# Kernel optimization log

Hardware: AMD Instinct MI355X
Metric: run time of the kernel (lower is better)

The kernel has to match this reference:

```python
import jax, jax.numpy as jnp
import numpy as np

B, C, H, W = 64, 256, 16, 16
HEADS, HEAD_DIM = 8, 256            # NOTE: source code requires H*W == HEAD_DIM
HID = HEADS * HEAD_DIM              # 2048
TEMB = 512
EPS = 1e-6
SC = HEAD_DIM ** -0.5


def setup_inputs() -> dict:
    key = jax.random.key(0)
    ks = jax.random.split(key, 6)
    return {
        "x": jax.random.normal(ks[0], (B, C, H, W), jnp.float32),
        "time_emb": jax.random.normal(ks[1], (B, TEMB), jnp.float32),
        "mlp_w": jax.random.normal(ks[2], (2 * C, TEMB), jnp.float32) * 0.02,
        "mlp_b": jnp.zeros((2 * C,), jnp.float32),
        "qkv_w": jax.random.normal(ks[3], (3 * HID, C), jnp.float32) * 0.02,
        "out_w": jax.random.normal(ks[4], (C, HID), jnp.float32) * 0.02,
        "out_b": jnp.zeros((C,), jnp.float32),
        "out_norm_scale": jnp.ones((C,), jnp.float32),
    }


def reference(x, time_emb, mlp_w, mlp_b, qkv_w, out_w, out_b, out_norm_scale):
    # AdaRMSNorm: SiLU -> Linear -> per-batch (scale, shift) over channels
    ss = jax.nn.silu(time_emb) @ mlp_w.T + mlp_b          # [B, 2C]
    scale, shift = jnp.split(ss, 2, axis=1)
    scale = scale[:, :, None, None]
    shift = shift[:, :, None, None]
    inv = jax.lax.rsqrt(jnp.mean(x * x, axis=1, keepdims=True) + EPS)
    xn = x * inv * (1.0 + scale) + shift

    # 1x1 conv producing q,k,v
    qkv = jnp.einsum('bchw,oc->bohw', xn, qkv_w)          # [B, 3*HID, H, W]
    q, k, v = jnp.split(qkv, 3, axis=1)

    def to_heads(t):
        return t.reshape(B, HEADS, HEAD_DIM, H * W)       # [B, h, d, L]

    q = jax.nn.softmax(to_heads(q), axis=2) * SC          # softmax over head_dim
    k = jax.nn.softmax(to_heads(k), axis=3)               # softmax over spatial
    v = to_heads(v)

    # Faithful to source einsums (contract over head_dim c, then over c and lw1)
    ctx = jnp.einsum('bhcn,bhcm->bhnm', k, v) * SC        # [B, h, L, L]
    out = jnp.einsum('bhnm,bhcl->bhml', ctx, q)           # [B, h, L, L]

    # rearrange 'b h c (l w) -> b (h c) l w' (valid since L == HEAD_DIM)
    out = out.reshape(B, HID, H, W)

    # output 1x1 conv + RMSNorm + residual
    y = jnp.einsum('bohw,co->bchw', out, out_w) + out_b[None, :, None, None]
    inv2 = jax.lax.rsqrt(jnp.mean(y * y, axis=1, keepdims=True) + EPS)
    y = y * inv2 * out_norm_scale[None, :, None, None]
    return y + x
```

## Files before the change

### kernel.cpp

```cpp
#include <hip/hip_runtime.h>
#include <math.h>


static constexpr float EPSV = 1e-6f;
static constexpr float SC2 = 1.0f / 256.0f;

__device__ __forceinline__ float wave_sum(float v) {
    v += __shfl_xor(v, 1);  v += __shfl_xor(v, 2);
    v += __shfl_xor(v, 4);  v += __shfl_xor(v, 8);
    v += __shfl_xor(v, 16); v += __shfl_xor(v, 32);
    return v;
}

__global__ void __launch_bounds__(256) k0_prep(
    const float* __restrict__ temb, const float* __restrict__ mlp_w,
    const float* __restrict__ mlp_b, const float* __restrict__ qkv_w,
    float* __restrict__ scsh, float* __restrict__ wvg)
{
    const int blk = blockIdx.x, tid = threadIdx.x;
    const int wv = tid >> 6, lane = tid & 63;
    if (blk < 1024) {
        int b = blk >> 4, jg = blk & 15;
        __shared__ float sl[512];
        float v0 = temb[b * 512 + tid];
        float v1 = temb[b * 512 + 256 + tid];
        sl[tid] = v0 / (1.0f + expf(-v0));
        sl[256 + tid] = v1 / (1.0f + expf(-v1));
        __syncthreads();
        int j0 = jg * 32 + wv * 8;
        float acc[8] = {0, 0, 0, 0, 0, 0, 0, 0};
        const float* wb = mlp_w + (size_t)j0 * 512 + lane;
#pragma unroll
        for (int k = 0; k < 8; ++k) {
            float sv = sl[k * 64 + lane];
#pragma unroll
            for (int jj = 0; jj < 8; ++jj)
                acc[jj] = fmaf(wb[(size_t)jj * 512 + k * 64], sv, acc[jj]);
        }
#pragma unroll
        for (int jj = 0; jj < 8; ++jj) {
            float a = wave_sum(acc[jj]);
            if (lane == 0) scsh[b * 512 + j0 + jj] = a + mlp_b[j0 + jj];
        }
    } else {
        int w = blk - 1024;
        int h = w >> 2, cq = w & 3;
        __shared__ float sm[256];
        const float* base =
            qkv_w + (size_t)(4096 + h * 256 + wv * 64) * 256 + cq * 64 + lane;
        float s = 0.f;
#pragma unroll 8
        for (int r = 0; r < 64; ++r) s += base[(size_t)r * 256];
        sm[wv * 64 + lane] = s;
        __syncthreads();
        if (tid < 64)
            wvg[h * 256 + cq * 64 + tid] =
                sm[tid] + sm[64 + tid] + sm[128 + tid] + sm[192 + tid];
    }
}

__global__ void __launch_bounds__(1024) k1_body(
    const float* __restrict__ x, const float* __restrict__ scsh,
    const float* __restrict__ wvg, const float* __restrict__ out_w,
    float* __restrict__ ypart)
{
    const int blk = blockIdx.x, tid = threadIdx.x;
    const int wv = tid >> 6, lane = tid & 63;
    const int b = blk >> 2, q = blk & 3;

    __shared__ float coef[256 * 8];
    __shared__ float apart[16 * 64 * 9];
    __shared__ float ofl[512];
    __shared__ float ssh[8];
    __shared__ float parts[4 * 8];

    if (tid < 256) {
        int c = tid;
        float sc = 1.0f + scsh[b * 512 + c];
        float sh = scsh[b * 512 + 256 + c];
#pragma unroll
        for (int h = 0; h < 8; ++h) {
            float wvv = wvg[h * 256 + c];
            coef[c * 8 + h] = sc * wvv;
            float sv = wave_sum(sh * wvv);
            if (lane == 0) parts[wv * 8 + h] = sv;
        }
    }
    __syncthreads();
    if (tid < 8)
        ssh[tid] = parts[tid] + parts[8 + tid] + parts[16 + tid] + parts[24 + tid];

    {
        int m = tid & 63, cg = tid >> 6;
        float A[8] = {0, 0, 0, 0, 0, 0, 0, 0};
        float ss2 = 0.f;
        const float* xb = x + (size_t)b * 65536 + q * 64 + m;
#pragma unroll
        for (int ci = 0; ci < 16; ++ci) {
            int c = cg * 16 + ci;
            float xv = xb[(size_t)c * 256];
            ss2 = fmaf(xv, xv, ss2);
            const float4 c0 = *reinterpret_cast<const float4*>(&coef[c * 8]);
            const float4 c1 = *reinterpret_cast<const float4*>(&coef[c * 8 + 4]);
            A[0] = fmaf(xv, c0.x, A[0]); A[1] = fmaf(xv, c0.y, A[1]);
            A[2] = fmaf(xv, c0.z, A[2]); A[3] = fmaf(xv, c0.w, A[3]);
            A[4] = fmaf(xv, c1.x, A[4]); A[5] = fmaf(xv, c1.y, A[5]);
            A[6] = fmaf(xv, c1.z, A[6]); A[7] = fmaf(xv, c1.w, A[7]);
        }
        float* ap = apart + ((size_t)(tid >> 6) * 64 + m) * 9;
#pragma unroll
        for (int h = 0; h < 8; ++h) ap[h] = A[h];
        ap[8] = ss2;
        (void)cg;
    }
    __syncthreads();
    if (tid < 64) {
        int m = tid;
        float fin[9] = {0, 0, 0, 0, 0, 0, 0, 0, 0};
#pragma unroll
        for (int g = 0; g < 16; ++g)
#pragma unroll
            for (int i = 0; i < 9; ++i)
                fin[i] += apart[((size_t)g * 64 + m) * 9 + i];
        float inv = rsqrtf(fin[8] * (1.0f / 256.0f) + EPSV);
#pragma unroll
        for (int h = 0; h < 8; ++h)
            ofl[h * 64 + m] = SC2 * fmaf(inv, fin[h], ssh[h]);
    }
    __syncthreads();

    const float4* of4 = reinterpret_cast<const float4*>(ofl);
#pragma unroll
    for (int g4 = 0; g4 < 4; ++g4) {
        int c0 = wv * 16 + g4 * 4;
        float a[4] = {0, 0, 0, 0};
#pragma unroll
        for (int cc = 0; cc < 4; ++cc) {
            int c = c0 + cc;
#pragma unroll
            for (int k = 0; k < 2; ++k) {
                int idx = k * 64 + lane;
                int h = idx >> 4, mm = (idx & 15) * 4;
                const float4 w4 = *reinterpret_cast<const float4*>(
                    &out_w[(size_t)c * 2048 + h * 256 + q * 64 + mm]);
                float4 ov = of4[idx];
                a[cc] = fmaf(w4.x, ov.x, a[cc]);
                a[cc] = fmaf(w4.y, ov.y, a[cc]);
                a[cc] = fmaf(w4.z, ov.z, a[cc]);
                a[cc] = fmaf(w4.w, ov.w, a[cc]);
            }
        }
#pragma unroll
        for (int cc = 0; cc < 4; ++cc) {
            float s = wave_sum(a[cc]);
            if (lane == 0) ypart[(size_t)q * 16384 + b * 256 + c0 + cc] = s;
        }
    }
}

__global__ void __launch_bounds__(256) k2_fin(
    const float* __restrict__ ypart, const float* __restrict__ out_b,
    const float* __restrict__ onorm, const float* __restrict__ x,
    float* __restrict__ out)
{
    const int blk = blockIdx.x, tid = threadIdx.x;
    const int b = blk >> 5, ch = blk & 31;
    __shared__ float gl[256];
    __shared__ float wred[4];
    float yb = out_b[tid] +
               ypart[b * 256 + tid] + ypart[16384 + b * 256 + tid] +
               ypart[32768 + b * 256 + tid] + ypart[49152 + b * 256 + tid];
    float v2 = wave_sum(yb * yb);
    if ((tid & 63) == 0) wred[tid >> 6] = v2;
    __syncthreads();
    float inv2 = rsqrtf((wred[0] + wred[1] + wred[2] + wred[3]) *
                        (1.0f / 256.0f) + EPSV);
    gl[tid] = yb * inv2 * onorm[tid];
    __syncthreads();

    const float4* xx = reinterpret_cast<const float4*>(x) +
                       (size_t)b * 16384 + ch * 512;
    float4* oo = reinterpret_cast<float4*>(out) + (size_t)b * 16384 + ch * 512;
#pragma unroll
    for (int k = 0; k < 2; ++k) {
        int i = k * 256 + tid;
        int row = (ch * 512 + i) >> 6;
        float4 xv = xx[i];
        float gg = gl[row];
        oo[i] = make_float4(xv.x + gg, xv.y + gg, xv.z + gg, xv.w + gg);
    }
}

extern "C" void kernel_launch(void* const* d_in, const int* in_sizes, int n_in,
                              void* d_out, int out_size, void* d_ws, size_t ws_size,
                              hipStream_t stream) {
    const float* x     = (const float*)d_in[0];
    const float* temb  = (const float*)d_in[1];
    const float* mlp_w = (const float*)d_in[2];
    const float* mlp_b = (const float*)d_in[3];
    const float* qkv_w = (const float*)d_in[4];
    const float* out_w = (const float*)d_in[5];
    const float* out_b = (const float*)d_in[6];
    const float* onorm = (const float*)d_in[7];
    float* out = (float*)d_out;
    float* ws  = (float*)d_ws;

    float* scsh  = ws;
    float* wvg   = ws + 32768;
    float* ypart = ws + 34816;

    k0_prep<<<1056, 256,  0, stream>>>(temb, mlp_w, mlp_b, qkv_w, scsh, wvg);
    k1_body<<<256,  1024, 0, stream>>>(x, scsh, wvg, out_w, ypart);
    k2_fin <<<2048, 256,  0, stream>>>(ypart, out_b, onorm, x, out);
}
```

Before: 35.02 us.

## Fuse three kernels into one persistent kernel with inter-block flag synchronization

Merges the prep, body and finalize kernels into a single 256-block launch. Blocks publish completion flags in workspace with release atomics and spin on them with acquire loads, replacing the kernel boundaries. A memset clears the flags before each launch. This removes two launch gaps and intermediate scheduling overhead, but the kernel depends on all 256 blocks being co-resident (otherwise it can deadlock), adds a memset, and loses parallelism in the prep and final phases.

Result: slower. 49.14 us (+40.3%).

```diff
diff --git a/kernel.cpp b/kernel.cpp
--- a/kernel.cpp
+++ b/kernel.cpp
@@ -4,6 +4,8 @@
 
 static constexpr float EPSV = 1e-6f;
 static constexpr float SC2 = 1.0f / 256.0f;
+
+#define NTHR 1024
 
 __device__ __forceinline__ float wave_sum(float v) {
     v += __shfl_xor(v, 1);  v += __shfl_xor(v, 2);
@@ -12,22 +14,40 @@
     return v;
 }
 
-__global__ void __launch_bounds__(256) k0_prep(
-    const float* __restrict__ temb, const float* __restrict__ mlp_w,
-    const float* __restrict__ mlp_b, const float* __restrict__ qkv_w,
-    float* __restrict__ scsh, float* __restrict__ wvg)
+__device__ __forceinline__ void rel_flag(unsigned* f) {
+    __hip_atomic_store(f, 1u, __ATOMIC_RELEASE, __HIP_MEMORY_SCOPE_AGENT);
+}
+__device__ __forceinline__ void spin_flag(unsigned* f) {
+    while (!__hip_atomic_load(f, __ATOMIC_RELAXED, __HIP_MEMORY_SCOPE_AGENT))
+        __builtin_amdgcn_s_sleep(1);
+    (void)__hip_atomic_load(f, __ATOMIC_ACQUIRE, __HIP_MEMORY_SCOPE_AGENT);
+}
+
+__global__ void __launch_bounds__(NTHR) k_all(
+    const float* __restrict__ x, const float* __restrict__ temb,
+    const float* __restrict__ mlp_w, const float* __restrict__ mlp_b,
+    const float* __restrict__ qkv_w, const float* __restrict__ out_w,
+    const float* __restrict__ out_b, const float* __restrict__ onorm,
+    float* __restrict__ out, float* __restrict__ ws)
 {
+    __shared__ float smem[12288];
+    unsigned* uf = (unsigned*)ws;
+    float* scsh  = ws + 16384;
+    float* wvg   = ws + 49152;
+    float* ypart = ws + 51200;
+
     const int blk = blockIdx.x, tid = threadIdx.x;
     const int wv = tid >> 6, lane = tid & 63;
-    if (blk < 1024) {
-        int b = blk >> 4, jg = blk & 15;
-        __shared__ float sl[512];
-        float v0 = temb[b * 512 + tid];
-        float v1 = temb[b * 512 + 256 + tid];
-        sl[tid] = v0 / (1.0f + expf(-v0));
-        sl[256 + tid] = v1 / (1.0f + expf(-v1));
-        __syncthreads();
-        int j0 = jg * 32 + wv * 8;
+    const int b = blk >> 2, q = blk & 3;
+
+    {
+        float* sl = smem;
+        if (tid < 512) {
+            float v = temb[b * 512 + tid];
+            sl[tid] = v / (1.0f + expf(-v));
+        }
+        __syncthreads();
+        int j0 = q * 128 + wv * 8;
         float acc[8] = {0, 0, 0, 0, 0, 0, 0, 0};
         const float* wb = mlp_w + (size_t)j0 * 512 + lane;
 #pragma unroll
@@ -42,37 +62,36 @@
             float a = wave_sum(acc[jj]);
             if (lane == 0) scsh[b * 512 + j0 + jj] = a + mlp_b[j0 + jj];
         }
-    } else {
-        int w = blk - 1024;
-        int h = w >> 2, cq = w & 3;
-        __shared__ float sm[256];
-        const float* base =
-            qkv_w + (size_t)(4096 + h * 256 + wv * 64) * 256 + cq * 64 + lane;
-        float s = 0.f;
-#pragma unroll 8
-        for (int r = 0; r < 64; ++r) s += base[(size_t)r * 256];
-        sm[wv * 64 + lane] = s;
-        __syncthreads();
-        if (tid < 64)
-            wvg[h * 256 + cq * 64 + tid] =
-                sm[tid] + sm[64 + tid] + sm[128 + tid] + sm[192 + tid];
-    }
-}
-
-__global__ void __launch_bounds__(1024) k1_body(
-    const float* __restrict__ x, const float* __restrict__ scsh,
-    const float* __restrict__ wvg, const float* __restrict__ out_w,
-    float* __restrict__ ypart)
-{
-    const int blk = blockIdx.x, tid = threadIdx.x;
-    const int wv = tid >> 6, lane = tid & 63;
-    const int b = blk >> 2, q = blk & 3;
-
-    __shared__ float coef[256 * 8];
-    __shared__ float apart[16 * 64 * 9];
-    __shared__ float ofl[512];
-    __shared__ float ssh[8];
-    __shared__ float parts[4 * 8];
+        if (blk < 32) {
+            int h = blk >> 2, cq = blk & 3;
+            float* wsum = smem + 512;
+            const float* base = qkv_w +
+                (size_t)(4096 + h * 256 + wv * 16) * 256 + cq * 64 + lane;
+            float s = 0.f;
+#pragma unroll
+            for (int r = 0; r < 16; ++r) s += base[(size_t)r * 256];
+            wsum[wv * 64 + lane] = s;
+            __syncthreads();
+            if (tid < 64) {
+                float t = 0.f;
+#pragma unroll
+                for (int r = 0; r < 16; ++r) t += wsum[r * 64 + tid];
+                wvg[h * 256 + cq * 64 + tid] = t;
+            }
+        }
+        __syncthreads();
+        if (tid == 0) rel_flag(uf + blk * 16);
+    }
+
+    if (tid < 4) spin_flag(uf + (b * 4 + tid) * 16);
+    else if (tid >= 64 && tid < 96) spin_flag(uf + (tid - 64) * 16);
+    __syncthreads();
+
+    float* coef  = smem;
+    float* apart = smem + 2048;
+    float* ofl   = smem + 11264;
+    float* ssh   = smem + 11776;
+    float* parts = smem + 11784;
 
     if (tid < 256) {
         int c = tid;
@@ -107,11 +126,10 @@
             A[4] = fmaf(xv, c1.x, A[4]); A[5] = fmaf(xv, c1.y, A[5]);
             A[6] = fmaf(xv, c1.z, A[6]); A[7] = fmaf(xv, c1.w, A[7]);
         }
-        float* ap = apart + ((size_t)(tid >> 6) * 64 + m) * 9;
+        float* ap = apart + ((size_t)cg * 64 + m) * 9;
 #pragma unroll
         for (int h = 0; h < 8; ++h) ap[h] = A[h];
         ap[8] = ss2;
-        (void)cg;
     }
     __syncthreads();
     if (tid < 64) {
@@ -129,65 +147,70 @@
     }
     __syncthreads();
 
-    const float4* of4 = reinterpret_cast<const float4*>(ofl);
-#pragma unroll
-    for (int g4 = 0; g4 < 4; ++g4) {
-        int c0 = wv * 16 + g4 * 4;
-        float a[4] = {0, 0, 0, 0};
-#pragma unroll
-        for (int cc = 0; cc < 4; ++cc) {
-            int c = c0 + cc;
-#pragma unroll
-            for (int k = 0; k < 2; ++k) {
-                int idx = k * 64 + lane;
-                int h = idx >> 4, mm = (idx & 15) * 4;
-                const float4 w4 = *reinterpret_cast<const float4*>(
-                    &out_w[(size_t)c * 2048 + h * 256 + q * 64 + mm]);
-                float4 ov = of4[idx];
-                a[cc] = fmaf(w4.x, ov.x, a[cc]);
-                a[cc] = fmaf(w4.y, ov.y, a[cc]);
-                a[cc] = fmaf(w4.z, ov.z, a[cc]);
-                a[cc] = fmaf(w4.w, ov.w, a[cc]);
+    {
+        const float4* of4 = reinterpret_cast<const float4*>(ofl);
+#pragma unroll
+        for (int g4 = 0; g4 < 4; ++g4) {
+            int c0 = wv * 16 + g4 * 4;
+            float a[4] = {0, 0, 0, 0};
+#pragma unroll
+            for (int cc = 0; cc < 4; ++cc) {
+                int c = c0 + cc;
+#pragma unroll
+                for (int k = 0; k < 2; ++k) {
+                    int idx = k * 64 + lane;
+                    int h = idx >> 4, mm = (idx & 15) * 4;
+                    const float4 w4 = *reinterpret_cast<const float4*>(
+                        &out_w[(size_t)c * 2048 + h * 256 + q * 64 + mm]);
+                    float4 ov = of4[idx];
+                    a[cc] = fmaf(w4.x, ov.x, a[cc]);
+                    a[cc] = fmaf(w4.y, ov.y, a[cc]);
+                    a[cc] = fmaf(w4.z, ov.z, a[cc]);
+                    a[cc] = fmaf(w4.w, ov.w, a[cc]);
+                }
             }
-        }
-#pragma unroll
-        for (int cc = 0; cc < 4; ++cc) {
-            float s = wave_sum(a[cc]);
-            if (lane == 0) ypart[(size_t)q * 16384 + b * 256 + c0 + cc] = s;
-        }
-    }
-}
-
-__global__ void __launch_bounds__(256) k2_fin(
-    const float* __restrict__ ypart, const float* __restrict__ out_b,
-    const float* __restrict__ onorm, const float* __restrict__ x,
-    float* __restrict__ out)
-{
-    const int blk = blockIdx.x, tid = threadIdx.x;
-    const int b = blk >> 5, ch = blk & 31;
-    __shared__ float gl[256];
-    __shared__ float wred[4];
-    float yb = out_b[tid] +
-               ypart[b * 256 + tid] + ypart[16384 + b * 256 + tid] +
-               ypart[32768 + b * 256 + tid] + ypart[49152 + b * 256 + tid];
-    float v2 = wave_sum(yb * yb);
-    if ((tid & 63) == 0) wred[tid >> 6] = v2;
-    __syncthreads();
-    float inv2 = rsqrtf((wred[0] + wred[1] + wred[2] + wred[3]) *
-                        (1.0f / 256.0f) + EPSV);
-    gl[tid] = yb * inv2 * onorm[tid];
-    __syncthreads();
-
-    const float4* xx = reinterpret_cast<const float4*>(x) +
-                       (size_t)b * 16384 + ch * 512;
-    float4* oo = reinterpret_cast<float4*>(out) + (size_t)b * 16384 + ch * 512;
-#pragma unroll
-    for (int k = 0; k < 2; ++k) {
-        int i = k * 256 + tid;
-        int row = (ch * 512 + i) >> 6;
-        float4 xv = xx[i];
-        float gg = gl[row];
-        oo[i] = make_float4(xv.x + gg, xv.y + gg, xv.z + gg, xv.w + gg);
+#pragma unroll
+            for (int cc = 0; cc < 4; ++cc) {
+                float s = wave_sum(a[cc]);
+                if (lane == 0)
+                    ypart[(size_t)q * 16384 + b * 256 + c0 + cc] = s;
+            }
+        }
+        __syncthreads();
+        if (tid == 0) rel_flag(uf + 4096 + blk * 16);
+    }
+
+    if (tid < 4) spin_flag(uf + 4096 + (b * 4 + tid) * 16);
+    __syncthreads();
+
+    {
+        float* g    = smem;
+        float* wred = smem + 320;
+        float yb = 0.f;
+        if (tid < 256) {
+            yb = out_b[tid] +
+                 ypart[b * 256 + tid] + ypart[16384 + b * 256 + tid] +
+                 ypart[32768 + b * 256 + tid] + ypart[49152 + b * 256 + tid];
+            float v2 = wave_sum(yb * yb);
+            if (lane == 0) wred[wv] = v2;
+        }
+        __syncthreads();
+        float inv2 = rsqrtf((wred[0] + wred[1] + wred[2] + wred[3]) *
+                            (1.0f / 256.0f) + EPSV);
+        if (tid < 256) g[tid] = yb * inv2 * onorm[tid];
+        __syncthreads();
+
+        const float4* xx = reinterpret_cast<const float4*>(x) + (size_t)b * 16384;
+        float4* oo = reinterpret_cast<float4*>(out) + (size_t)b * 16384;
+#pragma unroll
+        for (int r = 0; r < 4; ++r) {
+            int c = r * 64 + (tid >> 4);
+            int i = tid & 15;
+            size_t idx = (size_t)c * 64 + q * 16 + i;
+            float4 xv = xx[idx];
+            float gg = g[c];
+            oo[idx] = make_float4(xv.x + gg, xv.y + gg, xv.z + gg, xv.w + gg);
+        }
     }
 }
 
@@ -205,11 +228,7 @@
     float* out = (float*)d_out;
     float* ws  = (float*)d_ws;
 
-    float* scsh  = ws;
-    float* wvg   = ws + 32768;
-    float* ypart = ws + 34816;
-
-    k0_prep<<<1056, 256,  0, stream>>>(temb, mlp_w, mlp_b, qkv_w, scsh, wvg);
-    k1_body<<<256,  1024, 0, stream>>>(x, scsh, wvg, out_w, ypart);
-    k2_fin <<<2048, 256,  0, stream>>>(ypart, out_b, onorm, x, out);
-}
+    hipMemsetAsync(ws, 0, 32768, stream);
+    k_all<<<256, NTHR, 0, stream>>>(x, temb, mlp_w, mlp_b, qkv_w,
+                                    out_w, out_b, onorm, out, ws);
+}
```

## Fuse final RMSNorm and residual kernel into body kernel via inter-block flags

Applied to the files above, without the earlier changes.

Drops the separate finalize kernel. Each body block publishes its partial output-conv results, raises a release flag, then spins until the other three blocks of the same batch have done the same. It then computes the output RMSNorm and writes its quarter of the residual output. This removes one kernel launch and a round trip of the partials, but adds a hipMemsetAsync to clear the flags. It also relies on all 256 blocks being co-resident, or the spin-wait can deadlock.

After: 40.94 us. 16.9% more time.

```diff
diff --git a/kernel.cpp b/kernel.cpp
--- a/kernel.cpp
+++ b/kernel.cpp
@@ -10,6 +10,15 @@
     v += __shfl_xor(v, 4);  v += __shfl_xor(v, 8);
     v += __shfl_xor(v, 16); v += __shfl_xor(v, 32);
     return v;
+}
+
+__device__ __forceinline__ void rel_flag(unsigned* f) {
+    __hip_atomic_store(f, 1u, __ATOMIC_RELEASE, __HIP_MEMORY_SCOPE_AGENT);
+}
+__device__ __forceinline__ void spin_flag(unsigned* f) {
+    while (!__hip_atomic_load(f, __ATOMIC_RELAXED, __HIP_MEMORY_SCOPE_AGENT))
+        __builtin_amdgcn_s_sleep(1);
+    (void)__hip_atomic_load(f, __ATOMIC_ACQUIRE, __HIP_MEMORY_SCOPE_AGENT);
 }
 
 __global__ void __launch_bounds__(256) k0_prep(
@@ -62,11 +71,15 @@
 __global__ void __launch_bounds__(1024) k1_body(
     const float* __restrict__ x, const float* __restrict__ scsh,
     const float* __restrict__ wvg, const float* __restrict__ out_w,
-    float* __restrict__ ypart)
+    const float* __restrict__ out_b, const float* __restrict__ onorm,
+    float* __restrict__ out, float* __restrict__ ws)
 {
     const int blk = blockIdx.x, tid = threadIdx.x;
     const int wv = tid >> 6, lane = tid & 63;
     const int b = blk >> 2, q = blk & 3;
+
+    unsigned* uf = (unsigned*)ws;
+    float* ypart = ws + 4096;
 
     __shared__ float coef[256 * 8];
     __shared__ float apart[16 * 64 * 9];
@@ -107,11 +120,10 @@
             A[4] = fmaf(xv, c1.x, A[4]); A[5] = fmaf(xv, c1.y, A[5]);
             A[6] = fmaf(xv, c1.z, A[6]); A[7] = fmaf(xv, c1.w, A[7]);
         }
-        float* ap = apart + ((size_t)(tid >> 6) * 64 + m) * 9;
+        float* ap = apart + ((size_t)cg * 64 + m) * 9;
 #pragma unroll
         for (int h = 0; h < 8; ++h) ap[h] = A[h];
         ap[8] = ss2;
-        (void)cg;
     }
     __syncthreads();
     if (tid < 64) {
@@ -129,65 +141,70 @@
     }
     __syncthreads();
 
-    const float4* of4 = reinterpret_cast<const float4*>(ofl);
-#pragma unroll
-    for (int g4 = 0; g4 < 4; ++g4) {
-        int c0 = wv * 16 + g4 * 4;
-        float a[4] = {0, 0, 0, 0};
-#pragma unroll
-        for (int cc = 0; cc < 4; ++cc) {
-            int c = c0 + cc;
-#pragma unroll
-            for (int k = 0; k < 2; ++k) {
-                int idx = k * 64 + lane;
-                int h = idx >> 4, mm = (idx & 15) * 4;
-                const float4 w4 = *reinterpret_cast<const float4*>(
-                    &out_w[(size_t)c * 2048 + h * 256 + q * 64 + mm]);
-                float4 ov = of4[idx];
-                a[cc] = fmaf(w4.x, ov.x, a[cc]);
-                a[cc] = fmaf(w4.y, ov.y, a[cc]);
-                a[cc] = fmaf(w4.z, ov.z, a[cc]);
-                a[cc] = fmaf(w4.w, ov.w, a[cc]);
+    {
+        const float4* of4 = reinterpret_cast<const float4*>(ofl);
+#pragma unroll
+        for (int g4 = 0; g4 < 4; ++g4) {
+            int c0 = wv * 16 + g4 * 4;
+            float a[4] = {0, 0, 0, 0};
+#pragma unroll
+            for (int cc = 0; cc < 4; ++cc) {
+                int c = c0 + cc;
+#pragma unroll
+                for (int k = 0; k < 2; ++k) {
+                    int idx = k * 64 + lane;
+                    int h = idx >> 4, mm = (idx & 15) * 4;
+                    const float4 w4 = *reinterpret_cast<const float4*>(
+                        &out_w[(size_t)c * 2048 + h * 256 + q * 64 + mm]);
+                    float4 ov = of4[idx];
+                    a[cc] = fmaf(w4.x, ov.x, a[cc]);
+                    a[cc] = fmaf(w4.y, ov.y, a[cc]);
+                    a[cc] = fmaf(w4.z, ov.z, a[cc]);
+                    a[cc] = fmaf(w4.w, ov.w, a[cc]);
+                }
             }
-        }
-#pragma unroll
-        for (int cc = 0; cc < 4; ++cc) {
-            float s = wave_sum(a[cc]);
-            if (lane == 0) ypart[(size_t)q * 16384 + b * 256 + c0 + cc] = s;
-        }
-    }
-}
-
-__global__ void __launch_bounds__(256) k2_fin(
-    const float* __restrict__ ypart, const float* __restrict__ out_b,
-    const float* __restrict__ onorm, const float* __restrict__ x,
-    float* __restrict__ out)
-{
-    const int blk = blockIdx.x, tid = threadIdx.x;
-    const int b = blk >> 5, ch = blk & 31;
-    __shared__ float gl[256];
-    __shared__ float wred[4];
-    float yb = out_b[tid] +
-               ypart[b * 256 + tid] + ypart[16384 + b * 256 + tid] +
-               ypart[32768 + b * 256 + tid] + ypart[49152 + b * 256 + tid];
-    float v2 = wave_sum(yb * yb);
-    if ((tid & 63) == 0) wred[tid >> 6] = v2;
-    __syncthreads();
-    float inv2 = rsqrtf((wred[0] + wred[1] + wred[2] + wred[3]) *
-                        (1.0f / 256.0f) + EPSV);
-    gl[tid] = yb * inv2 * onorm[tid];
-    __syncthreads();
-
-    const float4* xx = reinterpret_cast<const float4*>(x) +
-                       (size_t)b * 16384 + ch * 512;
-    float4* oo = reinterpret_cast<float4*>(out) + (size_t)b * 16384 + ch * 512;
-#pragma unroll
-    for (int k = 0; k < 2; ++k) {
-        int i = k * 256 + tid;
-        int row = (ch * 512 + i) >> 6;
-        float4 xv = xx[i];
-        float gg = gl[row];
-        oo[i] = make_float4(xv.x + gg, xv.y + gg, xv.z + gg, xv.w + gg);
+#pragma unroll
+            for (int cc = 0; cc < 4; ++cc) {
+                float s = wave_sum(a[cc]);
+                if (lane == 0)
+                    ypart[(size_t)q * 16384 + b * 256 + c0 + cc] = s;
+            }
+        }
+    }
+    __syncthreads();
+    if (tid == 0) rel_flag(uf + blk * 16);
+
+    if (tid < 4) spin_flag(uf + (b * 4 + tid) * 16);
+    __syncthreads();
+
+    {
+        float* g    = coef;
+        float* wred = coef + 320;
+        float yb = 0.f;
+        if (tid < 256) {
+            yb = out_b[tid] +
+                 ypart[b * 256 + tid] + ypart[16384 + b * 256 + tid] +
+                 ypart[32768 + b * 256 + tid] + ypart[49152 + b * 256 + tid];
+            float v2 = wave_sum(yb * yb);
+            if (lane == 0) wred[wv] = v2;
+        }
+        __syncthreads();
+        float inv2 = rsqrtf((wred[0] + wred[1] + wred[2] + wred[3]) *
+                            (1.0f / 256.0f) + EPSV);
+        if (tid < 256) g[tid] = yb * inv2 * onorm[tid];
+        __syncthreads();
+
+        const float4* xx = reinterpret_cast<const float4*>(x) + (size_t)b * 16384;
+        float4* oo = reinterpret_cast<float4*>(out) + (size_t)b * 16384;
+#pragma unroll
+        for (int r = 0; r < 4; ++r) {
+            int c = r * 64 + (tid >> 4);
+            int i = tid & 15;
+            size_t idx = (size_t)c * 64 + q * 16 + i;
+            float4 xv = xx[idx];
+            float gg = g[c];
+            oo[idx] = make_float4(xv.x + gg, xv.y + gg, xv.z + gg, xv.w + gg);
+        }
     }
 }
 
@@ -205,11 +222,11 @@
     float* out = (float*)d_out;
     float* ws  = (float*)d_ws;
 
-    float* scsh  = ws;
-    float* wvg   = ws + 32768;
-    float* ypart = ws + 34816;
-
+    float* scsh = ws + 69632;
+    float* wvg  = ws + 102400;
+
+    hipMemsetAsync(ws, 0, 16384, stream);
     k0_prep<<<1056, 256,  0, stream>>>(temb, mlp_w, mlp_b, qkv_w, scsh, wvg);
-    k1_body<<<256,  1024, 0, stream>>>(x, scsh, wvg, out_w, ypart);
-    k2_fin <<<2048, 256,  0, stream>>>(ypart, out_b, onorm, x, out);
-}
+    k1_body<<<256,  1024, 0, stream>>>(x, scsh, wvg, out_w, out_b, onorm,
+                                       out, ws);
+}
```

## Split k1 body into 512 blocks over 32-column spatial chunks

Applied to the files above, without the earlier changes.

Doubles the k1 grid from 256 to 512 blocks by splitting each batch's spatial positions into 8 chunks of 32 instead of 4 chunks of 64. The channel reduction is reworked so 288 threads sum the partials in parallel instead of 64 threads doing it serially, and all 1024 threads now build the coefficient table. The output projection keeps each thread's ofl values in registers. The aim is to fill more compute units and cut the serial reduction, at the cost of more ypart partials for k2 to sum and more total reads of out_w.

Result: slower. 37.21 us (+6.3%).

```diff
diff --git a/kernel.cpp b/kernel.cpp
--- a/kernel.cpp
+++ b/kernel.cpp
@@ -66,38 +66,41 @@
 {
     const int blk = blockIdx.x, tid = threadIdx.x;
     const int wv = tid >> 6, lane = tid & 63;
-    const int b = blk >> 2, q = blk & 3;
+    const int b = blk >> 3, oc = blk & 7;
 
     __shared__ float coef[256 * 8];
-    __shared__ float apart[16 * 64 * 9];
-    __shared__ float ofl[512];
+    __shared__ float apart[32 * 32 * 9];
+    __shared__ float finbuf[32 * 9];
+    __shared__ float ofl[256];
     __shared__ float ssh[8];
-    __shared__ float parts[4 * 8];
-
-    if (tid < 256) {
-        int c = tid;
+    __shared__ float parts[8 * 4];
+
+    {
+        int c = tid & 255, hp = tid >> 8;
         float sc = 1.0f + scsh[b * 512 + c];
         float sh = scsh[b * 512 + 256 + c];
 #pragma unroll
-        for (int h = 0; h < 8; ++h) {
+        for (int e = 0; e < 2; ++e) {
+            int h = hp * 2 + e;
             float wvv = wvg[h * 256 + c];
             coef[c * 8 + h] = sc * wvv;
             float sv = wave_sum(sh * wvv);
-            if (lane == 0) parts[wv * 8 + h] = sv;
+            if (lane == 0) parts[h * 4 + (wv & 3)] = sv;
         }
     }
     __syncthreads();
     if (tid < 8)
-        ssh[tid] = parts[tid] + parts[8 + tid] + parts[16 + tid] + parts[24 + tid];
+        ssh[tid] = parts[tid * 4 + 0] + parts[tid * 4 + 1] +
+                   parts[tid * 4 + 2] + parts[tid * 4 + 3];
 
     {
-        int m = tid & 63, cg = tid >> 6;
+        int m = tid & 31, cg = tid >> 5;
         float A[8] = {0, 0, 0, 0, 0, 0, 0, 0};
         float ss2 = 0.f;
-        const float* xb = x + (size_t)b * 65536 + q * 64 + m;
-#pragma unroll
-        for (int ci = 0; ci < 16; ++ci) {
-            int c = cg * 16 + ci;
+        const float* xb = x + (size_t)b * 65536 + oc * 32 + m;
+#pragma unroll
+        for (int ci = 0; ci < 8; ++ci) {
+            int c = cg * 8 + ci;
             float xv = xb[(size_t)c * 256];
             ss2 = fmaf(xv, xv, ss2);
             const float4 c0 = *reinterpret_cast<const float4*>(&coef[c * 8]);
@@ -107,53 +110,54 @@
             A[4] = fmaf(xv, c1.x, A[4]); A[5] = fmaf(xv, c1.y, A[5]);
             A[6] = fmaf(xv, c1.z, A[6]); A[7] = fmaf(xv, c1.w, A[7]);
         }
-        float* ap = apart + ((size_t)(tid >> 6) * 64 + m) * 9;
+        float* ap = apart + ((size_t)cg * 32 + m) * 9;
 #pragma unroll
         for (int h = 0; h < 8; ++h) ap[h] = A[h];
         ap[8] = ss2;
-        (void)cg;
-    }
-    __syncthreads();
-    if (tid < 64) {
-        int m = tid;
-        float fin[9] = {0, 0, 0, 0, 0, 0, 0, 0, 0};
-#pragma unroll
-        for (int g = 0; g < 16; ++g)
-#pragma unroll
-            for (int i = 0; i < 9; ++i)
-                fin[i] += apart[((size_t)g * 64 + m) * 9 + i];
-        float inv = rsqrtf(fin[8] * (1.0f / 256.0f) + EPSV);
-#pragma unroll
-        for (int h = 0; h < 8; ++h)
-            ofl[h * 64 + m] = SC2 * fmaf(inv, fin[h], ssh[h]);
-    }
-    __syncthreads();
-
-    const float4* of4 = reinterpret_cast<const float4*>(ofl);
-#pragma unroll
-    for (int g4 = 0; g4 < 4; ++g4) {
-        int c0 = wv * 16 + g4 * 4;
-        float a[4] = {0, 0, 0, 0};
-#pragma unroll
-        for (int cc = 0; cc < 4; ++cc) {
-            int c = c0 + cc;
-#pragma unroll
-            for (int k = 0; k < 2; ++k) {
-                int idx = k * 64 + lane;
-                int h = idx >> 4, mm = (idx & 15) * 4;
+    }
+    __syncthreads();
+
+    if (tid < 288) {
+        int m = tid & 31, i = tid >> 5;
+        float s = 0.f;
+#pragma unroll
+        for (int cg = 0; cg < 32; ++cg)
+            s += apart[((size_t)cg * 32 + m) * 9 + i];
+        finbuf[m * 9 + i] = s;
+    }
+    __syncthreads();
+
+    if (tid < 256) {
+        int h = tid >> 5, m = tid & 31;
+        float inv = rsqrtf(finbuf[m * 9 + 8] * (1.0f / 256.0f) + EPSV);
+        ofl[h * 32 + m] = SC2 * fmaf(inv, finbuf[m * 9 + h], ssh[h]);
+    }
+    __syncthreads();
+
+    {
+        const float4* of4 = reinterpret_cast<const float4*>(ofl);
+        int h = lane >> 3, mm4 = lane & 7;
+        const float4 ov = of4[lane];
+        const size_t wbase = (size_t)h * 256 + oc * 32 + mm4 * 4;
+#pragma unroll
+        for (int g4 = 0; g4 < 4; ++g4) {
+            int c0 = wv * 16 + g4 * 4;
+            float a[4] = {0, 0, 0, 0};
+#pragma unroll
+            for (int cc = 0; cc < 4; ++cc) {
                 const float4 w4 = *reinterpret_cast<const float4*>(
-                    &out_w[(size_t)c * 2048 + h * 256 + q * 64 + mm]);
-                float4 ov = of4[idx];
+                    &out_w[(size_t)(c0 + cc) * 2048 + wbase]);
                 a[cc] = fmaf(w4.x, ov.x, a[cc]);
                 a[cc] = fmaf(w4.y, ov.y, a[cc]);
                 a[cc] = fmaf(w4.z, ov.z, a[cc]);
                 a[cc] = fmaf(w4.w, ov.w, a[cc]);
             }
-        }
-#pragma unroll
-        for (int cc = 0; cc < 4; ++cc) {
-            float s = wave_sum(a[cc]);
-            if (lane == 0) ypart[(size_t)q * 16384 + b * 256 + c0 + cc] = s;
+#pragma unroll
+            for (int cc = 0; cc < 4; ++cc) {
+                float s = wave_sum(a[cc]);
+                if (lane == 0)
+                    ypart[(size_t)oc * 16384 + b * 256 + c0 + cc] = s;
+            }
         }
     }
 }
@@ -167,9 +171,10 @@
     const int b = blk >> 5, ch = blk & 31;
     __shared__ float gl[256];
     __shared__ float wred[4];
-    float yb = out_b[tid] +
-               ypart[b * 256 + tid] + ypart[16384 + b * 256 + tid] +
-               ypart[32768 + b * 256 + tid] + ypart[49152 + b * 256 + tid];
+    float yb = out_b[tid];
+#pragma unroll
+    for (int oc = 0; oc < 8; ++oc)
+        yb += ypart[(size_t)oc * 16384 + b * 256 + tid];
     float v2 = wave_sum(yb * yb);
     if ((tid & 63) == 0) wred[tid >> 6] = v2;
     __syncthreads();
@@ -210,6 +215,6 @@
     float* ypart = ws + 34816;
 
     k0_prep<<<1056, 256,  0, stream>>>(temb, mlp_w, mlp_b, qkv_w, scsh, wvg);
-    k1_body<<<256,  1024, 0, stream>>>(x, scsh, wvg, out_w, ypart);
+    k1_body<<<512,  1024, 0, stream>>>(x, scsh, wvg, out_w, ypart);
     k2_fin <<<2048, 256,  0, stream>>>(ypart, out_b, onorm, x, out);
 }
```
